# Kernel tuning notes

Measured on AMD Instinct MI355X. Metric: run time of the kernel, lower is better.

## Reference

```python
import jax, jax.numpy as jnp
import numpy as np

HIDDEN = 1024
CUTOFFS = [20000, 80000, 200000]
PROJECT_FACTOR = 4
NUM_TAILS = len(CUTOFFS) - 1
CUTOFF_ENDS = [0] + CUTOFFS
BATCH, SEQ = 8, 1024


def _glorot(key, shape):
    fan_in, fan_out = shape
    limit = np.sqrt(6.0 / (fan_in + fan_out)).astype(np.float32)
    return jax.random.uniform(key, shape, jnp.float32, -limit, limit)


def setup_inputs() -> dict:
    key = jax.random.key(0)
    ks = jax.random.split(key, 7)
    return {
        "x": jax.random.randint(ks[0], (BATCH, SEQ), 0, CUTOFFS[-1], dtype=jnp.int64.dtype if jax.config.jax_enable_x64 else jnp.int32),
        "head_weight_proj": _glorot(ks[1], (HIDDEN, HIDDEN)),
        "head_weight": _glorot(ks[2], (HIDDEN, CUTOFFS[0] + NUM_TAILS)),
        "tail_weight_proj_0": _glorot(ks[3], (HIDDEN, HIDDEN // PROJECT_FACTOR)),
        "tail_weight_0": _glorot(ks[4], (HIDDEN // PROJECT_FACTOR, CUTOFFS[1] - CUTOFFS[0])),
        "tail_weight_proj_1": _glorot(ks[5], (HIDDEN, HIDDEN // PROJECT_FACTOR ** 2)),
        "tail_weight_1": _glorot(ks[6], (HIDDEN // PROJECT_FACTOR ** 2, CUTOFFS[2] - CUTOFFS[1])),
    }


def reference(x, head_weight_proj, head_weight, tail_weight_proj_0,
              tail_weight_0, tail_weight_proj_1, tail_weight_1) -> jnp.ndarray:
    # Faithful to AdaptiveEmbedding.compute_embeddings:
    #   tables[i] = weight.T (head truncated to cutoffs[0] rows), projs[i] = proj.T
    #   per-cluster: gather rows of table for in-range ids, matmul with proj,
    #   scatter back into y; here expressed densely with masks (same math,
    #   fixed shapes; out-of-cluster tokens contribute exactly zero).
    tables = [head_weight.T[:CUTOFFS[0]], tail_weight_0.T, tail_weight_1.T]
    projs = [head_weight_proj.T, tail_weight_proj_0.T, tail_weight_proj_1.T]
    y = jnp.zeros(x.shape + (HIDDEN,), dtype=jnp.float32)
    for i in range(len(CUTOFF_ENDS) - 1):
        l_idx, r_idx = CUTOFF_ENDS[i], CUTOFF_ENDS[i + 1]
        mask = (x >= l_idx) & (x < r_idx)                  # [B,S]
        idx = jnp.where(mask, x - l_idx, 0)                # in-range gather ids
        emb = tables[i][idx]                               # [B,S,d_i]
        proj = jnp.einsum('bsd,dh->bsh', emb, projs[i])    # [B,S,H]
        y = y + jnp.where(mask[..., None], proj, 0.0)
    emb_scale = jnp.asarray(HIDDEN ** 0.5, y.dtype)
    return y * emb_scale
```

## Files before the change

### kernel.cpp

```cpp
#include <hip/hip_runtime.h>
#include <hip/hip_bf16.h>

#define NTOK 8192
#define HID 1024
#define C0_END 20000
#define C1_END 80000
#define S0 20002
#define S1 60000
#define S2 120000

#define CAP0 1280
#define CAP1 3072
#define CAP2 6144
#define TS0 (CAP0/32)
#define TS1 (CAP1/32)
#define TS2 (CAP2/32)

#define NBUCK 12500

#define OFF_CNT 0
#define OFF_SST 16
#define OFF_LS  64
#define OFF_LI  (OFF_LS + NTOK*3*4)
#define OFF_W0  (OFF_LI + NTOK*3*4)
#define OFF_W1  (OFF_W0 + 1024*1024*2)
#define OFF_W2  (OFF_W1 + 256*1024*2)
#define OFF_A0  (OFF_W2 + 64*1024*2)
#define OFF_A1  (OFF_A0 + CAP0*1024*2)
#define OFF_A2  (OFF_A1 + CAP1*256*2)

typedef __attribute__((ext_vector_type(8))) short bf16x8;
typedef __attribute__((ext_vector_type(8))) unsigned short ushort8;
typedef __attribute__((ext_vector_type(4))) float f32x4;

__device__ __forceinline__ unsigned short f2bf(float f) {
    union { __hip_bfloat16 b; unsigned short u; } cv;
    cv.b = __float2bfloat16(f);
    return cv.u;
}

__global__ __launch_bounds__(1024) void k_pre(
        const int* __restrict__ x, int* __restrict__ cnt,
        unsigned* __restrict__ sstart, int* __restrict__ ls, int* __restrict__ li,
        const float* __restrict__ hwp, const float* __restrict__ twp0,
        const float* __restrict__ twp1,
        unsigned short* __restrict__ W0, unsigned short* __restrict__ W1,
        unsigned short* __restrict__ W2) {
    __shared__ unsigned hist[NBUCK];
    __shared__ unsigned psum[16];
    __shared__ unsigned sstl[3];
    if (blockIdx.x == 0) {
        int t = threadIdx.x, lane = t & 63, w = t >> 6;
        for (int i = t; i < NBUCK; i += 1024) hist[i] = 0u;
        __syncthreads();
        for (int i = t; i < NTOK; i += 1024)
            atomicAdd(&hist[x[i] >> 4], 1u);
        __syncthreads();
        int base = t * 13;
        unsigned loc[13];
        unsigned s = 0;
#pragma unroll
        for (int i = 0; i < 13; i++) {
            int idx = base + i;
            unsigned v = (idx < NBUCK) ? hist[idx] : 0u;
            loc[i] = v; s += v;
        }
        unsigned inc = s;
        for (int d = 1; d < 64; d <<= 1) {
            unsigned o = __shfl_up(inc, d);
            if (lane >= d) inc += o;
        }
        if (lane == 63) psum[w] = inc;
        __syncthreads();
        if (w == 0) {
            unsigned wsv = (lane < 16) ? psum[lane] : 0u;
            for (int d = 1; d < 16; d <<= 1) {
                unsigned o = __shfl_up(wsv, d);
                if (lane >= d) wsv += o;
            }
            if (lane < 16) psum[lane] = wsv;
        }
        __syncthreads();
        unsigned excl = inc - s + ((w > 0) ? psum[w - 1] : 0u);
#pragma unroll
        for (int i = 0; i < 13; i++) {
            int idx = base + i;
            if (idx < NBUCK) hist[idx] = excl;
            excl += loc[i];
        }
        __syncthreads();
        if (t == 0) {
            unsigned s1 = hist[1250], s2 = hist[5000];
            sstl[0] = 0u; sstl[1] = s1; sstl[2] = s2;
            sstart[0] = 0u; sstart[1] = s1; sstart[2] = s2;
            cnt[0] = (int)s1; cnt[1] = (int)(s2 - s1); cnt[2] = (int)(NTOK - s2);
        }
        __syncthreads();
        for (int i = t; i < NTOK; i += 1024) {
            int v = x[i];
            int c    = (v < C0_END) ? 0 : (v < C1_END ? 1 : 2);
            int bse  = (c == 0) ? 0 : (c == 1) ? C0_END : C1_END;
            unsigned cap = (c == 0) ? CAP0 : (c == 1) ? CAP1 : CAP2;
            unsigned pos = atomicAdd(&hist[v >> 4], 1u) - sstl[c];
            if (pos < cap) {
                ls[c * NTOK + pos] = i;
                li[c * NTOK + pos] = v - bse;
            }
        }
    } else {
        int gid = (blockIdx.x - 1) * 1024 + threadIdx.x;
        int stride = (gridDim.x - 1) * 1024;
        for (int i = gid; i < (1024 * 1024) / 4; i += stride) {
            float4 v = ((const float4*)hwp)[i];
            ushort4 o = { f2bf(v.x), f2bf(v.y), f2bf(v.z), f2bf(v.w) };
            ((ushort4*)W0)[i] = o;
        }
        for (int i = gid; i < (1024 * 256) / 4; i += stride) {
            float4 v = ((const float4*)twp0)[i];
            ushort4 o = { f2bf(v.x), f2bf(v.y), f2bf(v.z), f2bf(v.w) };
            ((ushort4*)W1)[i] = o;
        }
        for (int i = gid; i < (1024 * 64) / 4; i += stride) {
            float4 v = ((const float4*)twp1)[i];
            ushort4 o = { f2bf(v.x), f2bf(v.y), f2bf(v.z), f2bf(v.w) };
            ((ushort4*)W2)[i] = o;
        }
    }
}

template <int KS>
__device__ __forceinline__ size_t frag_off(int m, int k8) {
    return ((size_t)(((m >> 5) * KS + (k8 >> 2)) * 2 + ((m >> 4) & 1)) << 9)
         + (size_t)(((m & 15) + (k8 & 3) * 16) * 8);
}

template <int KS, int S, int MGSH>
__device__ __forceinline__ void spread_item(int e, int mi, int ki, int n,
                                            const float* __restrict__ t,
                                            const int* __restrict__ li,
                                            unsigned short* __restrict__ A) {
    int mg  = e >> MGSH;
    int k8g = e & ((1 << MGSH) - 1);
    int m  = mg * 8 + mi;
    int k8 = k8g * 8 + ki;
    int idx = (m < n) ? li[m] : 0;
    const float* src = t + (size_t)(k8 * 8) * S + idx;
    ushort8 v = {0, 0, 0, 0, 0, 0, 0, 0};
    if (m < n) {
#pragma unroll
        for (int j = 0; j < 8; j++) v[j] = f2bf(src[(size_t)j * S]);
    }
    *(ushort8*)(A + frag_off<KS>(m, k8)) = v;
}

__global__ void k_gather(const float* __restrict__ t0, const float* __restrict__ t1,
                         const float* __restrict__ t2,
                         const int* __restrict__ cnt, const int* __restrict__ li,
                         unsigned short* __restrict__ A0, unsigned short* __restrict__ A1,
                         unsigned short* __restrict__ A2) {
    int n0 = min(cnt[0], CAP0), n1 = min(cnt[1], CAP1), n2 = min(cnt[2], CAP2);
    int r0 = ((n0 + 31) >> 5) << 5;
    int r1 = ((n1 + 31) >> 5) << 5;
    int r2 = ((n2 + 31) >> 5) << 5;
    int i0 = r0 * 2;
    int i1 = r1 / 2;
    int i2 = r2 / 8;
    int tot = i0 + i1 + i2;
    int lane = threadIdx.x & 63;
    int mi = lane >> 3, ki = lane & 7;
    int wid = blockIdx.x * (blockDim.x >> 6) + (threadIdx.x >> 6);
    int nw  = gridDim.x * (blockDim.x >> 6);
    for (int it = wid; it < tot; it += nw) {
        if (it < i0)
            spread_item<32, S0, 4>(it, mi, ki, n0, t0, li, A0);
        else if (it < i0 + i1)
            spread_item<8, S1, 2>(it - i0, mi, ki, n1, t1, li + NTOK, A1);
        else
            spread_item<2, S2, 0>(it - i0 - i1, mi, ki, n2, t2, li + 2 * NTOK, A2);
    }
}

template <int K>
__device__ __forceinline__ void gemm_body(int tile, int n, int lane, int wave, int by,
                                          const unsigned short* __restrict__ Ap,
                                          const unsigned short* __restrict__ Wb,
                                          const int* __restrict__ ls,
                                          float* __restrict__ out) {
    constexpr int KS = K / 32;
    int m0 = tile * 32;
    int lr = lane & 15, lg = lane >> 4;
    int hb = by * 256 + wave * 64;
    const unsigned short* abase = Ap + (size_t)tile * KS * 1024 + lane * 8;
    const unsigned short* bbase = Wb + (size_t)(hb + lr) * K + lg * 8;
    f32x4 acc[2][4] = {};
#pragma unroll 4
    for (int ks = 0; ks < KS; ks++) {
        bf16x8 a0 = *(const bf16x8*)(abase + ks * 1024);
        bf16x8 a1 = *(const bf16x8*)(abase + ks * 1024 + 512);
        bf16x8 b0 = *(const bf16x8*)(bbase + ks * 32);
        bf16x8 b1 = *(const bf16x8*)(bbase + ks * 32 + 16 * K);
        bf16x8 b2 = *(const bf16x8*)(bbase + ks * 32 + 32 * K);
        bf16x8 b3 = *(const bf16x8*)(bbase + ks * 32 + 48 * K);
        acc[0][0] = __builtin_amdgcn_mfma_f32_16x16x32_bf16(a0, b0, acc[0][0], 0, 0, 0);
        acc[0][1] = __builtin_amdgcn_mfma_f32_16x16x32_bf16(a0, b1, acc[0][1], 0, 0, 0);
        acc[0][2] = __builtin_amdgcn_mfma_f32_16x16x32_bf16(a0, b2, acc[0][2], 0, 0, 0);
        acc[0][3] = __builtin_amdgcn_mfma_f32_16x16x32_bf16(a0, b3, acc[0][3], 0, 0, 0);
        acc[1][0] = __builtin_amdgcn_mfma_f32_16x16x32_bf16(a1, b0, acc[1][0], 0, 0, 0);
        acc[1][1] = __builtin_amdgcn_mfma_f32_16x16x32_bf16(a1, b1, acc[1][1], 0, 0, 0);
        acc[1][2] = __builtin_amdgcn_mfma_f32_16x16x32_bf16(a1, b2, acc[1][2], 0, 0, 0);
        acc[1][3] = __builtin_amdgcn_mfma_f32_16x16x32_bf16(a1, b3, acc[1][3], 0, 0, 0);
    }
#pragma unroll
    for (int mf = 0; mf < 2; mf++)
#pragma unroll
        for (int r = 0; r < 4; r++) {
            int m = mf * 16 + lg * 4 + r;
            if (m0 + m < n) {
                int s = ls[m0 + m];
                float* orow = out + (size_t)s * HID + hb + lr;
                orow[0]  = 32.f * acc[mf][0][r];
                orow[16] = 32.f * acc[mf][1][r];
                orow[32] = 32.f * acc[mf][2][r];
                orow[48] = 32.f * acc[mf][3][r];
            }
        }
}

__global__ __launch_bounds__(256) void k_gemm(const int* __restrict__ cnt,
                                              const int* __restrict__ ls,
                                              const unsigned short* __restrict__ A0,
                                              const unsigned short* __restrict__ A1,
                                              const unsigned short* __restrict__ A2,
                                              const unsigned short* __restrict__ W0,
                                              const unsigned short* __restrict__ W1,
                                              const unsigned short* __restrict__ W2,
                                              float* __restrict__ out) {
    int bx = blockIdx.x;
    int lane = threadIdx.x & 63, wave = threadIdx.x >> 6;
    if (bx < TS0) {
        int n = min(cnt[0], CAP0); if (bx * 32 >= n) return;
        gemm_body<1024>(bx, n, lane, wave, blockIdx.y, A0, W0, ls, out);
    } else if (bx < TS0 + TS1) {
        int t = bx - TS0;
        int n = min(cnt[1], CAP1); if (t * 32 >= n) return;
        gemm_body<256>(t, n, lane, wave, blockIdx.y, A1, W1, ls + NTOK, out);
    } else {
        int t = bx - TS0 - TS1;
        int n = min(cnt[2], CAP2); if (t * 32 >= n) return;
        gemm_body<64>(t, n, lane, wave, blockIdx.y, A2, W2, ls + 2 * NTOK, out);
    }
}

extern "C" void kernel_launch(void* const* d_in, const int* in_sizes, int n_in,
                              void* d_out, int out_size, void* d_ws, size_t ws_size,
                              hipStream_t stream) {
    const int*   x    = (const int*)d_in[0];
    const float* hwp  = (const float*)d_in[1];
    const float* hw   = (const float*)d_in[2];
    const float* twp0 = (const float*)d_in[3];
    const float* tw0  = (const float*)d_in[4];
    const float* twp1 = (const float*)d_in[5];
    const float* tw1  = (const float*)d_in[6];

    char* ws = (char*)d_ws;
    int* cnt          = (int*)(ws + OFF_CNT);
    unsigned* sstart  = (unsigned*)(ws + OFF_SST);
    int* ls           = (int*)(ws + OFF_LS);
    int* li           = (int*)(ws + OFF_LI);
    unsigned short* W0 = (unsigned short*)(ws + OFF_W0);
    unsigned short* W1 = (unsigned short*)(ws + OFF_W1);
    unsigned short* W2 = (unsigned short*)(ws + OFF_W2);
    unsigned short* A0 = (unsigned short*)(ws + OFF_A0);
    unsigned short* A1 = (unsigned short*)(ws + OFF_A1);
    unsigned short* A2 = (unsigned short*)(ws + OFF_A2);
    float* out = (float*)d_out;

    k_pre<<<257, 1024, 0, stream>>>(x, cnt, sstart, ls, li,
                                    hwp, twp0, twp1, W0, W1, W2);
    k_gather<<<1024, 256, 0, stream>>>(hw, tw0, tw1, cnt, li, A0, A1, A2);
    k_gemm<<<dim3(TS0 + TS1 + TS2, 4), 256, 0, stream>>>(
        cnt, ls, A0, A1, A2, W0, W1, W2, out);
}
```

Before: 72.32 us.

## Pipeline per-cluster gathers with previous cluster GEMMs across staged kernels

Splits the single gather kernel and single GEMM kernel into four launches. Each middle launch runs the GEMM for one cluster while other blocks gather the next cluster's rows, so memory-bound gathers overlap compute-bound MFMA work. The cost is two extra kernel launches and an imbalanced block split, where the gather portion gets whatever blocks remain after the GEMM tiles.

```diff
diff --git a/kernel.cpp b/kernel.cpp
--- a/kernel.cpp
+++ b/kernel.cpp
@@ -151,33 +151,6 @@
         for (int j = 0; j < 8; j++) v[j] = f2bf(src[(size_t)j * S]);
     }
     *(ushort8*)(A + frag_off<KS>(m, k8)) = v;
-}
-
-__global__ void k_gather(const float* __restrict__ t0, const float* __restrict__ t1,
-                         const float* __restrict__ t2,
-                         const int* __restrict__ cnt, const int* __restrict__ li,
-                         unsigned short* __restrict__ A0, unsigned short* __restrict__ A1,
-                         unsigned short* __restrict__ A2) {
-    int n0 = min(cnt[0], CAP0), n1 = min(cnt[1], CAP1), n2 = min(cnt[2], CAP2);
-    int r0 = ((n0 + 31) >> 5) << 5;
-    int r1 = ((n1 + 31) >> 5) << 5;
-    int r2 = ((n2 + 31) >> 5) << 5;
-    int i0 = r0 * 2;
-    int i1 = r1 / 2;
-    int i2 = r2 / 8;
-    int tot = i0 + i1 + i2;
-    int lane = threadIdx.x & 63;
-    int mi = lane >> 3, ki = lane & 7;
-    int wid = blockIdx.x * (blockDim.x >> 6) + (threadIdx.x >> 6);
-    int nw  = gridDim.x * (blockDim.x >> 6);
-    for (int it = wid; it < tot; it += nw) {
-        if (it < i0)
-            spread_item<32, S0, 4>(it, mi, ki, n0, t0, li, A0);
-        else if (it < i0 + i1)
-            spread_item<8, S1, 2>(it - i0, mi, ki, n1, t1, li + NTOK, A1);
-        else
-            spread_item<2, S2, 0>(it - i0 - i1, mi, ki, n2, t2, li + 2 * NTOK, A2);
-    }
 }
 
 template <int K>
@@ -226,29 +199,84 @@
         }
 }
 
-__global__ __launch_bounds__(256) void k_gemm(const int* __restrict__ cnt,
-                                              const int* __restrict__ ls,
-                                              const unsigned short* __restrict__ A0,
-                                              const unsigned short* __restrict__ A1,
-                                              const unsigned short* __restrict__ A2,
-                                              const unsigned short* __restrict__ W0,
-                                              const unsigned short* __restrict__ W1,
-                                              const unsigned short* __restrict__ W2,
-                                              float* __restrict__ out) {
-    int bx = blockIdx.x;
+__global__ __launch_bounds__(256) void k_g0(const float* __restrict__ t0,
+                                            const int* __restrict__ cnt,
+                                            const int* __restrict__ li,
+                                            unsigned short* __restrict__ A0) {
+    int n0 = min(cnt[0], CAP0);
+    int r0 = ((n0 + 31) >> 5) << 5;
+    int i0 = r0 * 2;
+    int lane = threadIdx.x & 63;
+    int mi = lane >> 3, ki = lane & 7;
+    int wid = blockIdx.x * 4 + (threadIdx.x >> 6);
+    int nw  = gridDim.x * 4;
+    for (int it = wid; it < i0; it += nw)
+        spread_item<32, S0, 4>(it, mi, ki, n0, t0, li, A0);
+}
+
+__global__ __launch_bounds__(256) void k_f1(const float* __restrict__ t1,
+                                            const int* __restrict__ cnt,
+                                            const int* __restrict__ li,
+                                            const int* __restrict__ ls,
+                                            const unsigned short* __restrict__ A0,
+                                            unsigned short* __restrict__ A1,
+                                            const unsigned short* __restrict__ W0,
+                                            float* __restrict__ out) {
+    int lane = threadIdx.x & 63;
+    if (blockIdx.x < TS0 * 4) {
+        int n0 = min(cnt[0], CAP0);
+        int tile = blockIdx.x >> 2, by = blockIdx.x & 3;
+        if (tile * 32 < n0)
+            gemm_body<1024>(tile, n0, lane, threadIdx.x >> 6, by, A0, W0, ls, out);
+    } else {
+        int n1 = min(cnt[1], CAP1);
+        int r1 = ((n1 + 31) >> 5) << 5;
+        int i1 = r1 / 2;
+        int mi = lane >> 3, ki = lane & 7;
+        int wid = (blockIdx.x - TS0 * 4) * 4 + (threadIdx.x >> 6);
+        int nw  = (gridDim.x - TS0 * 4) * 4;
+        for (int it = wid; it < i1; it += nw)
+            spread_item<8, S1, 2>(it, mi, ki, n1, t1, li + NTOK, A1);
+    }
+}
+
+__global__ __launch_bounds__(256) void k_f2(const float* __restrict__ t2,
+                                            const int* __restrict__ cnt,
+                                            const int* __restrict__ li,
+                                            const int* __restrict__ ls,
+                                            const unsigned short* __restrict__ A1,
+                                            unsigned short* __restrict__ A2,
+                                            const unsigned short* __restrict__ W1,
+                                            float* __restrict__ out) {
+    int lane = threadIdx.x & 63;
+    if (blockIdx.x < TS1 * 4) {
+        int n1 = min(cnt[1], CAP1);
+        int tile = blockIdx.x >> 2, by = blockIdx.x & 3;
+        if (tile * 32 < n1)
+            gemm_body<256>(tile, n1, lane, threadIdx.x >> 6, by, A1, W1,
+                           ls + NTOK, out);
+    } else {
+        int n2 = min(cnt[2], CAP2);
+        int r2 = ((n2 + 31) >> 5) << 5;
+        int i2 = r2 / 8;
+        int mi = lane >> 3, ki = lane & 7;
+        int wid = (blockIdx.x - TS1 * 4) * 4 + (threadIdx.x >> 6);
+        int nw  = (gridDim.x - TS1 * 4) * 4;
+        for (int it = wid; it < i2; it += nw)
+            spread_item<2, S2, 0>(it, mi, ki, n2, t2, li + 2 * NTOK, A2);
+    }
+}
+
+__global__ __launch_bounds__(256) void k_g2m(const int* __restrict__ cnt,
+                                             const int* __restrict__ ls,
+                                             const unsigned short* __restrict__ A2,
+                                             const unsigned short* __restrict__ W2,
+                                             float* __restrict__ out) {
+    int n2 = min(cnt[2], CAP2);
     int lane = threadIdx.x & 63, wave = threadIdx.x >> 6;
-    if (bx < TS0) {
-        int n = min(cnt[0], CAP0); if (bx * 32 >= n) return;
-        gemm_body<1024>(bx, n, lane, wave, blockIdx.y, A0, W0, ls, out);
-    } else if (bx < TS0 + TS1) {
-        int t = bx - TS0;
-        int n = min(cnt[1], CAP1); if (t * 32 >= n) return;
-        gemm_body<256>(t, n, lane, wave, blockIdx.y, A1, W1, ls + NTOK, out);
-    } else {
-        int t = bx - TS0 - TS1;
-        int n = min(cnt[2], CAP2); if (t * 32 >= n) return;
-        gemm_body<64>(t, n, lane, wave, blockIdx.y, A2, W2, ls + 2 * NTOK, out);
-    }
+    if (blockIdx.x * 32 < n2)
+        gemm_body<64>(blockIdx.x, n2, lane, wave, blockIdx.y, A2, W2,
+                      ls + 2 * NTOK, out);
 }
 
 extern "C" void kernel_launch(void* const* d_in, const int* in_sizes, int n_in,
@@ -277,7 +305,8 @@
 
     k_pre<<<257, 1024, 0, stream>>>(x, cnt, sstart, ls, li,
                                     hwp, twp0, twp1, W0, W1, W2);
-    k_gather<<<1024, 256, 0, stream>>>(hw, tw0, tw1, cnt, li, A0, A1, A2);
-    k_gemm<<<dim3(TS0 + TS1 + TS2, 4), 256, 0, stream>>>(
-        cnt, ls, A0, A1, A2, W0, W1, W2, out);
-}
+    k_g0<<<1024, 256, 0, stream>>>(hw, cnt, li, A0);
+    k_f1<<<1024, 256, 0, stream>>>(tw0, cnt, li, ls, A0, A1, W0, out);
+    k_f2<<<1024, 256, 0, stream>>>(tw1, cnt, li, ls, A1, A2, W1, out);
+    k_g2m<<<dim3(TS2, 4), 256, 0, stream>>>(cnt, ls, A2, W2, out);
+}
```

Measured after the change: 84.64 us. 1.17x slower.
